# Performance work log

Hardware: AMD Instinct MI355X
Metric: run time of the kernel (lower is better)

## Reference

```python
import jax, jax.numpy as jnp
import numpy as np

GAMMA = 0.5
ITERATIONS = 1


def setup_inputs() -> dict:
    key = jax.random.key(0)
    # x: [batch, heads, num_windows, N, dim]
    x = jax.random.normal(key, (4, 8, 64, 256, 128), dtype=jnp.float32)
    return {"x": x}


def _l2norm(v):
    return v / jnp.linalg.norm(v, axis=-1, keepdims=True)


def _get_codebook(x):
    # x: [b,h,w,n,d] -> c: [b,h,w,d]
    B, H, W, N, D = x.shape
    c = _l2norm(jnp.sum(x, axis=-2))              # init: window mean direction
    xf = x.reshape(B, H, W * N, D)                # flatten windows: [b,h,l,d], l = W*N
    for _ in range(ITERATIONS):
        aff = jnp.einsum('bhnd,bhld->bhnl', c, xf)           # [b,h,W,W*N]
        a_hw = jax.nn.one_hot(jnp.argmax(aff, axis=-1), W * N, dtype=x.dtype)  # [b,h,W,W*N]
        a_n = jax.nn.one_hot(jnp.argmax(aff, axis=-2), W, dtype=x.dtype)       # [b,h,W*N,W]
        attn = a_hw + jnp.swapaxes(a_n, -2, -1)              # [b,h,W,W*N]
        delta_c = _l2norm(jnp.einsum('bhnl,bhld->bhnd', attn, xf))
        c = _l2norm(GAMMA * c + (1.0 - GAMMA) * delta_c)
    return c


def reference(x):
    # x: [b,h,w,n,d]
    W = x.shape[2]
    c = _get_codebook(x)                                     # [b,h,w,d]
    cos_sim = jnp.einsum('bhrcd,bhsd->bhrcs', x, c)          # [b,h,w,n,w]
    delta_onehot = jax.nn.one_hot(jnp.argmax(cos_sim, axis=-1), W, dtype=jnp.float32)
    return delta_onehot, c
```

## Files before the change

kernel.cpp:

```cpp
#include <hip/hip_runtime.h>

typedef unsigned long long u64;
typedef unsigned int u32;

#define G_ 32
#define L_ 16384
#define D_ 128
#define ONEHOT_ 33554432LL

__global__ __launch_bounds__(256) void k1_sums(const float* __restrict__ x,
                                               float* __restrict__ c0n) {
  int blk = blockIdx.x;
  const float* xp = x + ((size_t)blk << 15);
  int t = threadIdx.x;
  int d4 = t & 31, r0 = t >> 5;
  float4 acc = make_float4(0.f, 0.f, 0.f, 0.f);
  #pragma unroll 4
  for (int r = r0; r < 256; r += 8) {
    float4 v = *(const float4*)(xp + r * D_ + d4 * 4);
    acc.x += v.x; acc.y += v.y; acc.z += v.z; acc.w += v.w;
  }
  __shared__ float4 part[8][32];
  __shared__ double ssq[33];
  part[r0][d4] = acc;
  __syncthreads();
  if (t < 32) {
    float4 s = part[0][t];
    for (int r = 1; r < 8; ++r) {
      float4 v = part[r][t];
      s.x += v.x; s.y += v.y; s.z += v.z; s.w += v.w;
    }
    part[0][t] = s;
    ssq[t] = (double)s.x * s.x + (double)s.y * s.y + (double)s.z * s.z + (double)s.w * s.w;
  }
  __syncthreads();
  if (t == 0) {
    double tot = 0.0;
    for (int i = 0; i < 32; ++i) tot += ssq[i];
    ssq[32] = 1.0 / sqrt(tot);
  }
  __syncthreads();
  if (t < 32) {
    float rn = (float)ssq[32];
    float4 s = part[0][t];
    float4 c = make_float4(s.x * rn, s.y * rn, s.z * rn, s.w * rn);
    *(float4*)(c0n + ((size_t)blk << 7) + t * 4) = c;
  }
}

__global__ __launch_bounds__(512)
void k2_assign(const float* __restrict__ x,
               const float* __restrict__ c0n,
               u32* __restrict__ aPack,
               u64* __restrict__ best) {
  __shared__ float4 cL[64 * 33];
  __shared__ float4 xq[8][16 * 9];
  int g = blockIdx.x >> 4, bsub = blockIdx.x & 15;
  int t = threadIdx.x, lane = t & 63, wv = t >> 6;
  int l15 = lane & 15, pg = lane >> 4;
  const float* xg = x + ((size_t)g << 21);
  const float4* cg4 = (const float4*)(c0n + ((size_t)g << 13));
  for (int i = t; i < 2048; i += 512)
    cL[(i >> 5) * 33 + (i & 31)] = cg4[i];
  __syncthreads();

  float4* xw = xq[wv];
  int sp = lane >> 2, sh = lane & 3;

  float rbv[4]; int rbp[4];
  #pragma unroll
  for (int s = 0; s < 4; ++s) { rbv[s] = -3.0e38f; rbp[s] = 0; }

  int wbase = bsub * 1024 + wv * 128;
  for (int tile = 0; tile < 8; ++tile) {
    int p0 = wbase + tile * 16;
    float4 acc[4][4];
    #pragma unroll
    for (int s = 0; s < 4; ++s)
      #pragma unroll
      for (int j = 0; j < 4; ++j) acc[s][j] = make_float4(0.f, 0.f, 0.f, 0.f);

    for (int q = 0; q < 4; ++q) {
      const float4* gsrc = (const float4*)(xg + ((size_t)(p0 + sp) << 7) + (q << 5));
      float4* xrow = xw + sp * 9;
      xrow[sh * 2]     = gsrc[sh * 2];
      xrow[sh * 2 + 1] = gsrc[sh * 2 + 1];
      #pragma unroll
      for (int d4l = 0; d4l < 8; ++d4l) {
        float4 ca[4];
        #pragma unroll
        for (int s = 0; s < 4; ++s)
          ca[s] = cL[(l15 + (s << 4)) * 33 + (q << 3) + d4l];
        #pragma unroll
        for (int j = 0; j < 4; ++j) {
          float4 xv = xw[(pg * 4 + j) * 9 + d4l];
          #pragma unroll
          for (int s = 0; s < 4; ++s) {
            acc[s][j].x += ca[s].x * xv.x;
            acc[s][j].y += ca[s].y * xv.y;
            acc[s][j].z += ca[s].z * xv.z;
            acc[s][j].w += ca[s].w * xv.w;
          }
        }
      }
    }

    int w1s[4];
    #pragma unroll
    for (int j = 0; j < 4; ++j) {
      int p = p0 + pg * 4 + j;
      float av[4];
      #pragma unroll
      for (int s = 0; s < 4; ++s)
        av[s] = (acc[s][j].x + acc[s][j].y) + (acc[s][j].z + acc[s][j].w);
      #pragma unroll
      for (int s = 0; s < 4; ++s)
        if (av[s] > rbv[s]) { rbv[s] = av[s]; rbp[s] = p; }
      float v1 = av[0]; int w1 = l15;
      #pragma unroll
      for (int s = 1; s < 4; ++s)
        if (av[s] > v1) { v1 = av[s]; w1 = l15 + (s << 4); }
      #pragma unroll
      for (int off = 1; off <= 8; off <<= 1) {
        float ov = __shfl_xor(v1, off); int ow = __shfl_xor(w1, off);
        if (ov > v1 || (ov == v1 && ow < w1)) { v1 = ov; w1 = ow; }
      }
      w1s[j] = w1;
    }

    if (l15 == 0) {
      u32 pk4 = (u32)w1s[0] | ((u32)w1s[1] << 8) |
                ((u32)w1s[2] << 16) | ((u32)w1s[3] << 24);
      aPack[((g * L_ + p0) >> 2) + pg] = pk4;
    }
  }

  #pragma unroll
  for (int s = 0; s < 4; ++s) {
    #pragma unroll
    for (int off = 16; off <= 32; off <<= 1) {
      float ov = __shfl_xor(rbv[s], off); int op = __shfl_xor(rbp[s], off);
      if (ov > rbv[s] || (ov == rbv[s] && op < rbp[s])) { rbv[s] = ov; rbp[s] = op; }
    }
  }
  if (pg == 0) {
    #pragma unroll
    for (int s = 0; s < 4; ++s) {
      u32 key = __float_as_uint(rbv[s]);
      key ^= (key & 0x80000000u) ? 0xFFFFFFFFu : 0x80000000u;
      u64 pk = ((u64)key << 32) | (u64)(0xFFFFFFFFu - (u32)rbp[s]);
      atomicMax(&best[(g << 6) + l15 + (s << 4)], pk);
    }
  }
}

__global__ __launch_bounds__(512)
void k2d_delta(const float* __restrict__ x,
               const u32* __restrict__ aPack,
               u64* __restrict__ deltaI) {
  __shared__ u64 ldsD[64 * 130];
  int g = blockIdx.x >> 4, bsub = blockIdx.x & 15;
  int t = threadIdx.x, lane = t & 63, wv = t >> 6;
  const float* xg = x + ((size_t)g << 21);
  for (int i = t; i < 64 * 130; i += 512) ldsD[i] = 0ULL;
  __syncthreads();

  int pbase = bsub * 1024 + wv * 128;
  #pragma unroll 4
  for (int i = 0; i < 128; ++i) {
    int p = pbase + i;
    u32 pk4 = aPack[(g * L_ + p) >> 2];
    int aw = (int)((pk4 >> ((p & 3) * 8)) & 63u);
    const float* xr = xg + ((size_t)p << 7);
    float va = xr[lane];
    float vb = xr[lane + 64];
    u64* dst = ldsD + aw * 130 + lane;
    atomicAdd(dst, (u64)(long long)__double2ll_rn((double)va * 4294967296.0));
    atomicAdd(dst + 64, (u64)(long long)__double2ll_rn((double)vb * 4294967296.0));
  }

  __syncthreads();
  for (int i = t; i < 8192; i += 512) {
    u64 v = ldsD[(i >> 7) * 130 + (i & 127)];
    if (v) atomicAdd(&deltaI[((size_t)g << 13) + i], v);
  }
}

__global__ __launch_bounds__(128) void k3_final(const float* __restrict__ x,
                                                const float* __restrict__ c0n,
                                                const u64* __restrict__ deltaI,
                                                const u64* __restrict__ best,
                                                float* __restrict__ cOut,
                                                float* __restrict__ c2n) {
  int blk = blockIdx.x, g = blk >> 6;
  int d = threadIdx.x;
  u64 pk = best[blk];
  int bl = (int)(0xFFFFFFFFu - (u32)(pk & 0xFFFFFFFFull));
  float xb = x[((size_t)g << 21) + ((size_t)bl << 7) + d];
  long long di = (long long)deltaI[((size_t)blk << 7) + d];
  double delta = (double)di * (1.0 / 4294967296.0) + (double)xb;

  __shared__ double red[128];
  __shared__ double inv;
  red[d] = delta * delta;
  __syncthreads();
  for (int s = 64; s > 0; s >>= 1) {
    if (d < s) red[d] += red[d + s];
    __syncthreads();
  }
  if (d == 0) inv = 1.0 / sqrt(red[0]);
  __syncthreads();
  float dn = (float)(delta * inv);
  float b2 = 0.5f * c0n[((size_t)blk << 7) + d] + 0.5f * dn;
  __syncthreads();
  red[d] = (double)b2 * b2;
  __syncthreads();
  for (int s = 64; s > 0; s >>= 1) {
    if (d < s) red[d] += red[d + s];
    __syncthreads();
  }
  if (d == 0) inv = 1.0 / sqrt(red[0]);
  __syncthreads();
  float cf = b2 * (float)inv;
  cOut[((size_t)blk << 7) + d] = cf;
  c2n[((size_t)blk << 7) + d] = cf;
}

__global__ __launch_bounds__(512)
void k4_onehot(const float* __restrict__ x,
               const float* __restrict__ c2n,
               float* __restrict__ out) {
  __shared__ float4 cL[64 * 33];
  __shared__ float4 xq[8][16 * 9];
  int g = blockIdx.x >> 4, bsub = blockIdx.x & 15;
  int t = threadIdx.x, lane = t & 63, wv = t >> 6;
  int l15 = lane & 15, pg = lane >> 4;
  const float* xg = x + ((size_t)g << 21);
  const float4* cg4 = (const float4*)(c2n + ((size_t)g << 13));
  for (int i = t; i < 2048; i += 512)
    cL[(i >> 5) * 33 + (i & 31)] = cg4[i];
  __syncthreads();

  float4* xw = xq[wv];
  int sp = lane >> 2, sh = lane & 3;

  int wbase = bsub * 1024 + wv * 128;
  for (int tile = 0; tile < 8; ++tile) {
    int p0 = wbase + tile * 16;
    float4 acc[4][4];
    #pragma unroll
    for (int s = 0; s < 4; ++s)
      #pragma unroll
      for (int j = 0; j < 4; ++j) acc[s][j] = make_float4(0.f, 0.f, 0.f, 0.f);

    for (int q = 0; q < 4; ++q) {
      const float4* gsrc = (const float4*)(xg + ((size_t)(p0 + sp) << 7) + (q << 5));
      float4* xrow = xw + sp * 9;
      xrow[sh * 2]     = gsrc[sh * 2];
      xrow[sh * 2 + 1] = gsrc[sh * 2 + 1];
      #pragma unroll
      for (int d4l = 0; d4l < 8; ++d4l) {
        float4 ca[4];
        #pragma unroll
        for (int s = 0; s < 4; ++s)
          ca[s] = cL[(l15 + (s << 4)) * 33 + (q << 3) + d4l];
        #pragma unroll
        for (int j = 0; j < 4; ++j) {
          float4 xv = xw[(pg * 4 + j) * 9 + d4l];
          #pragma unroll
          for (int s = 0; s < 4; ++s) {
            acc[s][j].x += ca[s].x * xv.x;
            acc[s][j].y += ca[s].y * xv.y;
            acc[s][j].z += ca[s].z * xv.z;
            acc[s][j].w += ca[s].w * xv.w;
          }
        }
      }
    }

    #pragma unroll
    for (int j = 0; j < 4; ++j) {
      int p = p0 + pg * 4 + j;
      float av[4];
      #pragma unroll
      for (int s = 0; s < 4; ++s)
        av[s] = (acc[s][j].x + acc[s][j].y) + (acc[s][j].z + acc[s][j].w);
      float v1 = av[0]; int w1 = l15;
      #pragma unroll
      for (int s = 1; s < 4; ++s)
        if (av[s] > v1) { v1 = av[s]; w1 = l15 + (s << 4); }
      #pragma unroll
      for (int off = 1; off <= 8; off <<= 1) {
        float ov = __shfl_xor(v1, off); int ow = __shfl_xor(w1, off);
        if (ov > v1 || (ov == v1 && ow < w1)) { v1 = ov; w1 = ow; }
      }
      int w0 = l15 << 2;
      float4 vv;
      vv.x = (w1 == w0    ) ? 1.f : 0.f;
      vv.y = (w1 == w0 + 1) ? 1.f : 0.f;
      vv.z = (w1 == w0 + 2) ? 1.f : 0.f;
      vv.w = (w1 == w0 + 3) ? 1.f : 0.f;
      *(float4*)(out + (((size_t)(g * L_ + p)) << 6) + w0) = vv;
    }
  }
}

extern "C" void kernel_launch(void* const* d_in, const int* in_sizes, int n_in,
                              void* d_out, int out_size, void* d_ws, size_t ws_size,
                              hipStream_t stream) {
  const float* x = (const float*)d_in[0];
  float* out = (float*)d_out;
  float* cOut = out + ONEHOT_;
  char* ws = (char*)d_ws;
  float* c0n   = (float*)(ws);
  float* c2n   = (float*)(ws + (1u << 20));
  u64*  deltaI = (u64*)(ws + (3u << 20));
  u64*  best   = (u64*)(ws + (5u << 20));
  u32*  aPack  = (u32*)(ws + (5u << 20) + 65536);

  hipMemsetAsync(ws + (3u << 20), 0, (2u << 20) + 16384, stream);

  hipLaunchKernelGGL(k1_sums,   dim3(2048), dim3(256), 0, stream, x, c0n);
  hipLaunchKernelGGL(k2_assign, dim3(512),  dim3(512), 0, stream, x, c0n, aPack, best);
  hipLaunchKernelGGL(k2d_delta, dim3(512),  dim3(512), 0, stream, x, aPack, deltaI);
  hipLaunchKernelGGL(k3_final,  dim3(2048), dim3(128), 0, stream,
                     x, c0n, deltaI, best, cOut, c2n);
  hipLaunchKernelGGL(k4_onehot, dim3(512),  dim3(512), 0, stream, x, c2n, out);
}
```

Baseline: 489.9 us.

## Double-buffer x tiles via async global_load_lds with XOR-swizzled LDS layout

In the assign and onehot kernels, x tiles were loaded synchronously through registers into padded LDS rows. They are now fetched with 16-byte global_load_lds instructions straight into a per-wave double buffer. The next stage is issued before computing on the current one, with vmcnt waits gating its use. This is meant to overlap global memory latency with the FMA work and remove the register round-trip. The padded layout is replaced by an XOR swizzle to avoid LDS bank conflicts. The change costs more LDS per block and relies on correct manual vmcnt accounting.

```diff
diff --git a/kernel.cpp b/kernel.cpp
--- a/kernel.cpp
+++ b/kernel.cpp
@@ -7,6 +7,27 @@
 #define L_ 16384
 #define D_ 128
 #define ONEHOT_ 33554432LL
+
+__device__ inline void gload16(const float* g, float* lds) {
+  __builtin_amdgcn_global_load_lds(
+      (const __attribute__((address_space(1))) unsigned int*)g,
+      (__attribute__((address_space(3))) unsigned int*)lds, 16, 0, 0);
+}
+
+__device__ inline void issue_stage(const float* xg, float4* xw, int wbase,
+                                   int nq, int lane) {
+  int tb = wbase + ((nq >> 2) << 4);
+  int qq = nq & 3;
+  float4* dst = xw + ((nq & 1) << 7);
+  #pragma unroll
+  for (int k = 0; k < 2; ++k) {
+    int idx = (k << 6) + lane;
+    int p = idx >> 3, d4s = idx & 7;
+    int d4 = d4s ^ ((p >> 2) << 1);
+    const float* src = xg + ((size_t)(tb + p) << 7) + (qq << 5) + (d4 << 2);
+    gload16(src, (float*)(dst + (k << 6)));
+  }
+}
 
 __global__ __launch_bounds__(256) void k1_sums(const float* __restrict__ x,
                                                float* __restrict__ c0n) {
@@ -54,7 +75,7 @@
                u32* __restrict__ aPack,
                u64* __restrict__ best) {
   __shared__ float4 cL[64 * 33];
-  __shared__ float4 xq[8][16 * 9];
+  __shared__ float4 xq[8][256];
   int g = blockIdx.x >> 4, bsub = blockIdx.x & 15;
   int t = threadIdx.x, lane = t & 63, wv = t >> 6;
   int l15 = lane & 15, pg = lane >> 4;
@@ -65,13 +86,14 @@
   __syncthreads();
 
   float4* xw = xq[wv];
-  int sp = lane >> 2, sh = lane & 3;
 
   float rbv[4]; int rbp[4];
   #pragma unroll
   for (int s = 0; s < 4; ++s) { rbv[s] = -3.0e38f; rbp[s] = 0; }
 
   int wbase = bsub * 1024 + wv * 128;
+  issue_stage(xg, xw, wbase, 0, lane);
+
   for (int tile = 0; tile < 8; ++tile) {
     int p0 = wbase + tile * 16;
     float4 acc[4][4];
@@ -81,10 +103,14 @@
       for (int j = 0; j < 4; ++j) acc[s][j] = make_float4(0.f, 0.f, 0.f, 0.f);
 
     for (int q = 0; q < 4; ++q) {
-      const float4* gsrc = (const float4*)(xg + ((size_t)(p0 + sp) << 7) + (q << 5));
-      float4* xrow = xw + sp * 9;
-      xrow[sh * 2]     = gsrc[sh * 2];
-      xrow[sh * 2 + 1] = gsrc[sh * 2 + 1];
+      int qi = (tile << 2) + q;
+      if (qi < 31) {
+        issue_stage(xg, xw, wbase, qi + 1, lane);
+        asm volatile("s_waitcnt vmcnt(2)" ::: "memory");
+      } else {
+        asm volatile("s_waitcnt vmcnt(0)" ::: "memory");
+      }
+      const float4* xb = xw + ((q & 1) << 7);
       #pragma unroll
       for (int d4l = 0; d4l < 8; ++d4l) {
         float4 ca[4];
@@ -93,7 +119,7 @@
           ca[s] = cL[(l15 + (s << 4)) * 33 + (q << 3) + d4l];
         #pragma unroll
         for (int j = 0; j < 4; ++j) {
-          float4 xv = xw[(pg * 4 + j) * 9 + d4l];
+          float4 xv = xb[((pg << 2) + j) * 8 + (d4l ^ (pg << 1))];
           #pragma unroll
           for (int s = 0; s < 4; ++s) {
             acc[s][j].x += ca[s].x * xv.x;
@@ -231,7 +257,7 @@
                const float* __restrict__ c2n,
                float* __restrict__ out) {
   __shared__ float4 cL[64 * 33];
-  __shared__ float4 xq[8][16 * 9];
+  __shared__ float4 xq[8][256];
   int g = blockIdx.x >> 4, bsub = blockIdx.x & 15;
   int t = threadIdx.x, lane = t & 63, wv = t >> 6;
   int l15 = lane & 15, pg = lane >> 4;
@@ -242,9 +268,9 @@
   __syncthreads();
 
   float4* xw = xq[wv];
-  int sp = lane >> 2, sh = lane & 3;
-
   int wbase = bsub * 1024 + wv * 128;
+  issue_stage(xg, xw, wbase, 0, lane);
+
   for (int tile = 0; tile < 8; ++tile) {
     int p0 = wbase + tile * 16;
     float4 acc[4][4];
@@ -254,10 +280,14 @@
       for (int j = 0; j < 4; ++j) acc[s][j] = make_float4(0.f, 0.f, 0.f, 0.f);
 
     for (int q = 0; q < 4; ++q) {
-      const float4* gsrc = (const float4*)(xg + ((size_t)(p0 + sp) << 7) + (q << 5));
-      float4* xrow = xw + sp * 9;
-      xrow[sh * 2]     = gsrc[sh * 2];
-      xrow[sh * 2 + 1] = gsrc[sh * 2 + 1];
+      int qi = (tile << 2) + q;
+      if (qi < 31) {
+        issue_stage(xg, xw, wbase, qi + 1, lane);
+        asm volatile("s_waitcnt vmcnt(2)" ::: "memory");
+      } else {
+        asm volatile("s_waitcnt vmcnt(0)" ::: "memory");
+      }
+      const float4* xb = xw + ((q & 1) << 7);
       #pragma unroll
       for (int d4l = 0; d4l < 8; ++d4l) {
         float4 ca[4];
@@ -266,7 +296,7 @@
           ca[s] = cL[(l15 + (s << 4)) * 33 + (q << 3) + d4l];
         #pragma unroll
         for (int j = 0; j < 4; ++j) {
-          float4 xv = xw[(pg * 4 + j) * 9 + d4l];
+          float4 xv = xb[((pg << 2) + j) * 8 + (d4l ^ (pg << 1))];
           #pragma unroll
           for (int s = 0; s < 4; ++s) {
             acc[s][j].x += ca[s].x * xv.x;
```

Result: slower. 853.5 us (+74.2%).
